# Kernel optimization log

Hardware: AMD Instinct MI355X
Metric: run time of the kernel (lower is better)

## Reference

```python
import jax, jax.numpy as jnp
import numpy as np

DIM = 768
NUM_HEADS = 12
HEAD_DIM = DIM // NUM_HEADS
SCALE = HEAD_DIM ** -0.5


def setup_inputs() -> dict:
    key = jax.random.key(0)
    k_x, k_qkv, k_proj, k_pb = jax.random.split(key, 4)
    B, N = 8, 1024
    x = jax.random.normal(k_x, (B, N, DIM), dtype=jnp.float32)
    # nn.Linear(dim, 3*dim, bias=False): weight [3*dim, dim]
    w_qkv = jax.random.normal(k_qkv, (3 * DIM, DIM), dtype=jnp.float32) * (DIM ** -0.5)
    # nn.Linear(dim, dim): weight [dim, dim], bias [dim]
    w_proj = jax.random.normal(k_proj, (DIM, DIM), dtype=jnp.float32) * (DIM ** -0.5)
    b_proj = jax.random.normal(k_pb, (DIM,), dtype=jnp.float32) * 0.01
    return {"x": x, "w_qkv": w_qkv, "w_proj": w_proj, "b_proj": b_proj}


def reference(x, w_qkv, w_proj, b_proj):
    B, N, C = x.shape
    H, D = NUM_HEADS, HEAD_DIM
    # qkv: [B, N, 3C] -> [3, B, H, N, D]
    qkv = jnp.einsum('bnc,oc->bno', x, w_qkv)
    qkv = qkv.reshape(B, N, 3, H, D).transpose(2, 0, 3, 1, 4)
    q, k, v = qkv[0], qkv[1], qkv[2]
    # scores in float32 (module explicitly casts to float)
    attn = jnp.einsum('bhnd,bhmd->bhnm', q.astype(jnp.float32), k.astype(jnp.float32)) * SCALE
    attn = jax.nn.softmax(attn, axis=-1)
    attn = jnp.where(jnp.isnan(attn), 0.0, attn)  # masked_fill nan -> 0
    out = jnp.einsum('bhnm,bhmd->bhnd', attn, v.astype(jnp.float32))
    out = out.transpose(0, 2, 1, 3).reshape(B, N, C)
    out = jnp.einsum('bnc,oc->bno', out, w_proj) + b_proj
    return out
```

## Files before the change

kernel.cpp:

```cpp
#include <hip/hip_runtime.h>

typedef _Float16 half8 __attribute__((ext_vector_type(8)));
typedef _Float16 half4 __attribute__((ext_vector_type(4)));
typedef float f32x4 __attribute__((ext_vector_type(4)));

#define NHEAD 12
#define HDIM  64
#define SEQ   1024
#define CDIM  768
#define O3    2304
#define MTOK  8192

__device__ __forceinline__ void load_lds16(const void* g, void* l) {
  __builtin_amdgcn_global_load_lds(
      (const __attribute__((address_space(1))) unsigned int*)g,
      (__attribute__((address_space(3))) unsigned int*)l, 16, 0, 0);
}

__global__ __launch_bounds__(256) void cast_f2h(const float* __restrict__ in,
                                                _Float16* __restrict__ out) {
  size_t i = ((size_t)blockIdx.x * 256 + threadIdx.x) * 4;
  float4 v = *reinterpret_cast<const float4*>(in + i);
  half4 h;
  h[0] = (_Float16)v.x; h[1] = (_Float16)v.y; h[2] = (_Float16)v.z; h[3] = (_Float16)v.w;
  *reinterpret_cast<half4*>(out + i) = h;
}

__global__ __launch_bounds__(256) void qkv_gemm(const _Float16* __restrict__ A,
                                                const _Float16* __restrict__ Bw,
                                                _Float16* __restrict__ Qh,
                                                _Float16* __restrict__ Kh,
                                                _Float16* __restrict__ VT) {
  __shared__ _Float16 As[2][128 * 32];
  __shared__ _Float16 Bs[2][128 * 32];
  const int tid  = threadIdx.x;
  const int lane = tid & 63;
  const int wv   = tid >> 6;
  const int wm   = wv >> 1;
  const int wn   = wv & 1;
  const int fr   = lane & 15;
  const int kg   = lane >> 4;

  const int lin = blockIdx.y * gridDim.x + blockIdx.x;
  const int cpx = (gridDim.x * gridDim.y) >> 3;
  const int swz = (lin & 7) * cpx + (lin >> 3);
  const int m0  = (swz / 18) * 128;
  const int n0  = (swz % 18) * 128;

  f32x4 acc[4][4];
#pragma unroll
  for (int i = 0; i < 4; ++i)
#pragma unroll
    for (int j = 0; j < 4; ++j) acc[i][j] = (f32x4){0.f, 0.f, 0.f, 0.f};

  auto stage = [&](int buf, int kt) {
#pragma unroll
    for (int r = 0; r < 2; ++r) {
      const int c = r * 256 + tid;
      const int row = c >> 2, cc = c & 3;
      load_lds16(A + (size_t)(m0 + row) * CDIM + kt + ((cc ^ (row & 3)) * 8),
                 &As[buf][c * 8]);
    }
#pragma unroll
    for (int r = 0; r < 2; ++r) {
      const int c = r * 256 + tid;
      const int row = c >> 2, cc = c & 3;
      load_lds16(Bw + (size_t)(n0 + row) * CDIM + kt + ((cc ^ (row & 3)) * 8),
                 &Bs[buf][c * 8]);
    }
  };

  int cur = 0;
  stage(0, 0);
  __syncthreads();

  for (int it = 0; it < 24; ++it) {
    if (it + 1 < 24) stage(cur ^ 1, (it + 1) * 32);
    half8 a[4], b[4];
#pragma unroll
    for (int i = 0; i < 4; ++i) {
      const int row = wm * 64 + i * 16 + fr;
      a[i] = *reinterpret_cast<half8*>(&As[cur][row * 32 + ((kg ^ (row & 3)) * 8)]);
    }
#pragma unroll
    for (int j = 0; j < 4; ++j) {
      const int row = wn * 64 + j * 16 + fr;
      b[j] = *reinterpret_cast<half8*>(&Bs[cur][row * 32 + ((kg ^ (row & 3)) * 8)]);
    }
#pragma unroll
    for (int i = 0; i < 4; ++i)
#pragma unroll
      for (int j = 0; j < 4; ++j)
        acc[i][j] = __builtin_amdgcn_mfma_f32_16x16x32_f16(a[i], b[j], acc[i][j], 0, 0, 0);
    if (it + 1 < 24) {
      __syncthreads();
      cur ^= 1;
    }
  }

  const int t     = n0 / CDIM;
  const int hbase = n0 - t * CDIM;
#pragma unroll
  for (int i = 0; i < 4; ++i) {
    const int mrow = m0 + wm * 64 + i * 16 + kg * 4;
#pragma unroll
    for (int j = 0; j < 4; ++j) {
      const int hd = hbase + wn * 64 + j * 16 + fr;
      const int h  = hd >> 6, d = hd & 63;
#pragma unroll
      for (int r = 0; r < 4; ++r) {
        const int m  = mrow + r;
        const int bb = m >> 10, nn = m & 1023;
        const float v = acc[i][j][r];
        if (t == 0)
          Qh[(((size_t)(bb * NHEAD + h)) << 16) + (nn << 6) + d] = (_Float16)(v * 0.125f);
        else if (t == 1)
          Kh[(((size_t)(bb * NHEAD + h)) << 16) + (nn << 6) + d] = (_Float16)v;
        else
          VT[(((size_t)(bb * NHEAD + h)) << 16) + (d << 10) + nn] = (_Float16)v;
      }
    }
  }
}

__global__ __launch_bounds__(256) void attn_kernel(const _Float16* __restrict__ Qh,
                                                   const _Float16* __restrict__ Kh,
                                                   const _Float16* __restrict__ VT,
                                                   _Float16* __restrict__ AO) {
  __shared__ _Float16 Ks[64 * 64];
  __shared__ _Float16 Vs[64 * 64];
  __shared__ _Float16 Ps[4 * 16 * 64];
  const int tid  = threadIdx.x;
  const int lane = tid & 63;
  const int w    = tid >> 6;
  const int fr   = lane & 15;
  const int kg   = lane >> 4;
  const int kh   = kg * 8;
  const int bh   = blockIdx.x;
  const int qt   = blockIdx.y;
  const int q0   = qt * 64 + w * 16;
  const size_t qkbase = (size_t)bh * SEQ * HDIM;
  char* const psw = (char*)&Ps[w * 16 * 64];

  half8 qb[2];
#pragma unroll
  for (int ks = 0; ks < 2; ++ks)
    qb[ks] = *reinterpret_cast<const half8*>(
        &Qh[qkbase + (size_t)(q0 + fr) * HDIM + ks * 32 + kh]);

  f32x4 O[4];
  float mrun = -__builtin_inff();
  float lrun = 0.f;
#pragma unroll
  for (int fd = 0; fd < 4; ++fd) O[fd] = (f32x4){0.f, 0.f, 0.f, 0.f};

  for (int kt = 0; kt < SEQ; kt += 64) {
    __syncthreads();
#pragma unroll
    for (int r = 0; r < 2; ++r) {
      const int c = r * 256 + tid;
      const int row = c >> 3, cc = c & 7;
      load_lds16(&Kh[qkbase + (size_t)(kt + row) * HDIM + ((cc ^ (row & 7)) * 8)], &Ks[c * 8]);
    }
#pragma unroll
    for (int r = 0; r < 2; ++r) {
      const int c = r * 256 + tid;
      const int row = c >> 3, cc = c & 7;
      load_lds16(&VT[(size_t)bh * HDIM * SEQ + (size_t)row * SEQ + kt + ((cc ^ (row & 7)) * 8)],
                 &Vs[c * 8]);
    }
    __syncthreads();

    f32x4 st[4];
#pragma unroll
    for (int fc = 0; fc < 4; ++fc) st[fc] = (f32x4){0.f, 0.f, 0.f, 0.f};
#pragma unroll
    for (int ks = 0; ks < 2; ++ks) {
#pragma unroll
      for (int fc = 0; fc < 4; ++fc) {
        const int row = fc * 16 + fr;
        const int colh = ks * 32 + kh;
        half8 ka = *reinterpret_cast<half8*>(&Ks[row * 64 + (((colh >> 3) ^ (row & 7)) << 3)]);
        st[fc] = __builtin_amdgcn_mfma_f32_16x16x32_f16(ka, qb[ks], st[fc], 0, 0, 0);
      }
    }

    float mx = st[0][0];
#pragma unroll
    for (int fc = 0; fc < 4; ++fc)
#pragma unroll
      for (int r = 0; r < 4; ++r) mx = fmaxf(mx, st[fc][r]);
    mx = fmaxf(mx, __shfl_xor(mx, 16));
    mx = fmaxf(mx, __shfl_xor(mx, 32));
    const float mnew = fmaxf(mrun, mx);
    const float corr = __expf(mrun - mnew);
    mrun = mnew;
    float rs = 0.f;
#pragma unroll
    for (int fc = 0; fc < 4; ++fc)
#pragma unroll
      for (int r = 0; r < 4; ++r) {
        const float p = __expf(st[fc][r] - mnew);
        st[fc][r] = p;
        rs += p;
      }
    rs += __shfl_xor(rs, 16);
    rs += __shfl_xor(rs, 32);
    lrun = lrun * corr + rs;

#pragma unroll
    for (int r = 0; r < 4; ++r) {
      const float c4 = __shfl(corr, kg * 4 + r);
#pragma unroll
      for (int fd = 0; fd < 4; ++fd) O[fd][r] *= c4;
    }

#pragma unroll
    for (int fc = 0; fc < 4; ++fc) {
      half4 pk;
      pk[0] = (_Float16)st[fc][0];
      pk[1] = (_Float16)st[fc][1];
      pk[2] = (_Float16)st[fc][2];
      pk[3] = (_Float16)st[fc][3];
      const int slot = (fc * 2 + (kg >> 1)) ^ (fr & 7);
      *reinterpret_cast<half4*>(psw + fr * 128 + slot * 16 + (kg & 1) * 8) = pk;
    }

#pragma unroll
    for (int ks = 0; ks < 2; ++ks) {
      const int rslot = (ks * 4 + kg) ^ (fr & 7);
      half8 pa = *reinterpret_cast<half8*>(psw + fr * 128 + rslot * 16);
#pragma unroll
      for (int fd = 0; fd < 4; ++fd) {
        const int row = fd * 16 + fr;
        const int colh = ks * 32 + kh;
        half8 vb = *reinterpret_cast<half8*>(&Vs[row * 64 + (((colh >> 3) ^ (row & 7)) << 3)]);
        O[fd] = __builtin_amdgcn_mfma_f32_16x16x32_f16(pa, vb, O[fd], 0, 0, 0);
      }
    }
  }

  const int b = bh / NHEAD, h = bh % NHEAD;
  const float linv = 1.0f / lrun;
#pragma unroll
  for (int r = 0; r < 4; ++r) {
    const float lq = __shfl(linv, kg * 4 + r);
    const int n = q0 + kg * 4 + r;
#pragma unroll
    for (int fd = 0; fd < 4; ++fd)
      AO[((size_t)b * SEQ + n) * CDIM + h * HDIM + fd * 16 + fr] =
          (_Float16)(O[fd][r] * lq);
  }
}

__global__ __launch_bounds__(256) void proj_gemm(const _Float16* __restrict__ A,
                                                 const _Float16* __restrict__ Bw,
                                                 const float* __restrict__ bias,
                                                 float* __restrict__ Out) {
  __shared__ _Float16 As[2][128 * 32];
  __shared__ _Float16 Bs[2][128 * 32];
  const int tid  = threadIdx.x;
  const int lane = tid & 63;
  const int wv   = tid >> 6;
  const int wm   = wv >> 1;
  const int wn   = wv & 1;
  const int fr   = lane & 15;
  const int kg   = lane >> 4;

  const int lin = blockIdx.y * gridDim.x + blockIdx.x;
  const int cpx = (gridDim.x * gridDim.y) >> 3;
  const int swz = (lin & 7) * cpx + (lin >> 3);
  const int m0  = (swz / 6) * 128;
  const int n0  = (swz % 6) * 128;

  f32x4 acc[4][4];
#pragma unroll
  for (int i = 0; i < 4; ++i)
#pragma unroll
    for (int j = 0; j < 4; ++j) acc[i][j] = (f32x4){0.f, 0.f, 0.f, 0.f};

  auto stage = [&](int buf, int kt) {
#pragma unroll
    for (int r = 0; r < 2; ++r) {
      const int c = r * 256 + tid;
      const int row = c >> 2, cc = c & 3;
      load_lds16(A + (size_t)(m0 + row) * CDIM + kt + ((cc ^ (row & 3)) * 8),
                 &As[buf][c * 8]);
    }
#pragma unroll
    for (int r = 0; r < 2; ++r) {
      const int c = r * 256 + tid;
      const int row = c >> 2, cc = c & 3;
      load_lds16(Bw + (size_t)(n0 + row) * CDIM + kt + ((cc ^ (row & 3)) * 8),
                 &Bs[buf][c * 8]);
    }
  };

  int cur = 0;
  stage(0, 0);
  __syncthreads();

  for (int it = 0; it < 24; ++it) {
    if (it + 1 < 24) stage(cur ^ 1, (it + 1) * 32);
    half8 a[4], b[4];
#pragma unroll
    for (int i = 0; i < 4; ++i) {
      const int row = wm * 64 + i * 16 + fr;
      a[i] = *reinterpret_cast<half8*>(&As[cur][row * 32 + ((kg ^ (row & 3)) * 8)]);
    }
#pragma unroll
    for (int j = 0; j < 4; ++j) {
      const int row = wn * 64 + j * 16 + fr;
      b[j] = *reinterpret_cast<half8*>(&Bs[cur][row * 32 + ((kg ^ (row & 3)) * 8)]);
    }
#pragma unroll
    for (int i = 0; i < 4; ++i)
#pragma unroll
      for (int j = 0; j < 4; ++j)
        acc[i][j] = __builtin_amdgcn_mfma_f32_16x16x32_f16(a[i], b[j], acc[i][j], 0, 0, 0);
    if (it + 1 < 24) {
      __syncthreads();
      cur ^= 1;
    }
  }

#pragma unroll
  for (int i = 0; i < 4; ++i) {
    const int mrow = m0 + wm * 64 + i * 16 + kg * 4;
#pragma unroll
    for (int j = 0; j < 4; ++j) {
      const int ocol = n0 + wn * 64 + j * 16 + fr;
      const float bv = bias[ocol];
#pragma unroll
      for (int r = 0; r < 4; ++r)
        Out[(size_t)(mrow + r) * CDIM + ocol] = acc[i][j][r] + bv;
    }
  }
}

extern "C" void kernel_launch(void* const* d_in, const int* in_sizes, int n_in,
                              void* d_out, int out_size, void* d_ws, size_t ws_size,
                              hipStream_t stream) {
  const float* x     = (const float*)d_in[0];
  const float* wqkv  = (const float*)d_in[1];
  const float* wproj = (const float*)d_in[2];
  const float* bproj = (const float*)d_in[3];
  float* out = (float*)d_out;

  char* ws = (char*)d_ws;
  _Float16* x_h     = (_Float16*)(ws);
  _Float16* wqkv_h  = (_Float16*)(ws + 12582912);
  _Float16* wproj_h = (_Float16*)(ws + 16121856);
  _Float16* Qh      = (_Float16*)(ws + 17301504);
  _Float16* Kh      = (_Float16*)(ws + 29884416);
  _Float16* VT      = (_Float16*)(ws + 42467328);
  _Float16* AOh     = (_Float16*)(ws + 55050240);

  cast_f2h<<<6291456 / 1024, 256, 0, stream>>>(x, x_h);
  cast_f2h<<<1769472 / 1024, 256, 0, stream>>>(wqkv, wqkv_h);
  cast_f2h<<<589824 / 1024, 256, 0, stream>>>(wproj, wproj_h);

  qkv_gemm<<<dim3(O3 / 128, MTOK / 128), 256, 0, stream>>>(x_h, wqkv_h, Qh, Kh, VT);
  attn_kernel<<<dim3(96, 16), 256, 0, stream>>>(Qh, Kh, VT, AOh);
  proj_gemm<<<dim3(CDIM / 128, MTOK / 128), 256, 0, stream>>>(AOh, wproj_h, bproj, out);
}
```

Before: 164.9 us.

## Double-buffer K/V tiles in attention and widen GEMM K-tiles to 64

The attention kernel now keeps two LDS buffers for K and V and loads the next tile while computing on the current one, where before every tile load was bracketed by barriers with no overlap. The QKV and projection GEMMs move from a 32-wide to a 64-wide K step with an 8-way XOR swizzle and named ping-pong buffers, which halves the number of barriers per output tile. This doubles LDS use per block in all three kernels, which may lower occupancy.

New measurement: 144.0 us. 12.7% less time.

```diff
diff --git a/kernel.cpp b/kernel.cpp
--- a/kernel.cpp
+++ b/kernel.cpp
@@ -31,8 +31,8 @@
                                                 _Float16* __restrict__ Qh,
                                                 _Float16* __restrict__ Kh,
                                                 _Float16* __restrict__ VT) {
-  __shared__ _Float16 As[2][128 * 32];
-  __shared__ _Float16 Bs[2][128 * 32];
+  __shared__ _Float16 As0[128 * 64], Bs0[128 * 64];
+  __shared__ _Float16 As1[128 * 64], Bs1[128 * 64];
   const int tid  = threadIdx.x;
   const int lane = tid & 63;
   const int wv   = tid >> 6;
@@ -53,49 +53,55 @@
 #pragma unroll
     for (int j = 0; j < 4; ++j) acc[i][j] = (f32x4){0.f, 0.f, 0.f, 0.f};
 
-  auto stage = [&](int buf, int kt) {
-#pragma unroll
-    for (int r = 0; r < 2; ++r) {
-      const int c = r * 256 + tid;
-      const int row = c >> 2, cc = c & 3;
-      load_lds16(A + (size_t)(m0 + row) * CDIM + kt + ((cc ^ (row & 3)) * 8),
-                 &As[buf][c * 8]);
-    }
-#pragma unroll
-    for (int r = 0; r < 2; ++r) {
-      const int c = r * 256 + tid;
-      const int row = c >> 2, cc = c & 3;
-      load_lds16(Bw + (size_t)(n0 + row) * CDIM + kt + ((cc ^ (row & 3)) * 8),
-                 &Bs[buf][c * 8]);
-    }
-  };
-
-  int cur = 0;
-  stage(0, 0);
+  auto stage = [&](_Float16* Ad, _Float16* Bd, int kt) {
+#pragma unroll
+    for (int r = 0; r < 4; ++r) {
+      const int c = r * 256 + tid;
+      const int row = c >> 3, cc = c & 7;
+      load_lds16(A + (size_t)(m0 + row) * CDIM + kt + ((cc ^ (row & 7)) * 8), Ad + c * 8);
+    }
+#pragma unroll
+    for (int r = 0; r < 4; ++r) {
+      const int c = r * 256 + tid;
+      const int row = c >> 3, cc = c & 7;
+      load_lds16(Bw + (size_t)(n0 + row) * CDIM + kt + ((cc ^ (row & 7)) * 8), Bd + c * 8);
+    }
+  };
+
+  auto compute = [&](const _Float16* As, const _Float16* Bs) {
+#pragma unroll
+    for (int kk = 0; kk < 2; ++kk) {
+      half8 a[4], b[4];
+#pragma unroll
+      for (int i = 0; i < 4; ++i) {
+        const int row = wm * 64 + i * 16 + fr;
+        a[i] = *reinterpret_cast<const half8*>(
+            &As[row * 64 + (((kk * 4 + kg) ^ (row & 7)) * 8)]);
+      }
+#pragma unroll
+      for (int j = 0; j < 4; ++j) {
+        const int row = wn * 64 + j * 16 + fr;
+        b[j] = *reinterpret_cast<const half8*>(
+            &Bs[row * 64 + (((kk * 4 + kg) ^ (row & 7)) * 8)]);
+      }
+#pragma unroll
+      for (int i = 0; i < 4; ++i)
+#pragma unroll
+        for (int j = 0; j < 4; ++j)
+          acc[i][j] = __builtin_amdgcn_mfma_f32_16x16x32_f16(a[i], b[j], acc[i][j], 0, 0, 0);
+    }
+  };
+
+  stage(As0, Bs0, 0);
   __syncthreads();
-
-  for (int it = 0; it < 24; ++it) {
-    if (it + 1 < 24) stage(cur ^ 1, (it + 1) * 32);
-    half8 a[4], b[4];
-#pragma unroll
-    for (int i = 0; i < 4; ++i) {
-      const int row = wm * 64 + i * 16 + fr;
-      a[i] = *reinterpret_cast<half8*>(&As[cur][row * 32 + ((kg ^ (row & 3)) * 8)]);
-    }
-#pragma unroll
-    for (int j = 0; j < 4; ++j) {
-      const int row = wn * 64 + j * 16 + fr;
-      b[j] = *reinterpret_cast<half8*>(&Bs[cur][row * 32 + ((kg ^ (row & 3)) * 8)]);
-    }
-#pragma unroll
-    for (int i = 0; i < 4; ++i)
-#pragma unroll
-      for (int j = 0; j < 4; ++j)
-        acc[i][j] = __builtin_amdgcn_mfma_f32_16x16x32_f16(a[i], b[j], acc[i][j], 0, 0, 0);
-    if (it + 1 < 24) {
-      __syncthreads();
-      cur ^= 1;
-    }
+  for (int it = 0; it < 6; ++it) {
+    const int kt = it * 128;
+    stage(As1, Bs1, kt + 64);
+    compute(As0, Bs0);
+    __syncthreads();
+    if (kt + 128 < CDIM) stage(As0, Bs0, kt + 128);
+    compute(As1, Bs1);
+    __syncthreads();
   }
 
   const int t     = n0 / CDIM;
@@ -127,8 +133,8 @@
                                                    const _Float16* __restrict__ Kh,
                                                    const _Float16* __restrict__ VT,
                                                    _Float16* __restrict__ AO) {
-  __shared__ _Float16 Ks[64 * 64];
-  __shared__ _Float16 Vs[64 * 64];
+  __shared__ _Float16 Ks0[64 * 64], Vs0[64 * 64];
+  __shared__ _Float16 Ks1[64 * 64], Vs1[64 * 64];
   __shared__ _Float16 Ps[4 * 16 * 64];
   const int tid  = threadIdx.x;
   const int lane = tid & 63;
@@ -154,23 +160,23 @@
 #pragma unroll
   for (int fd = 0; fd < 4; ++fd) O[fd] = (f32x4){0.f, 0.f, 0.f, 0.f};
 
-  for (int kt = 0; kt < SEQ; kt += 64) {
-    __syncthreads();
+  auto stageKV = [&](_Float16* Kd, _Float16* Vd, int kt) {
 #pragma unroll
     for (int r = 0; r < 2; ++r) {
       const int c = r * 256 + tid;
       const int row = c >> 3, cc = c & 7;
-      load_lds16(&Kh[qkbase + (size_t)(kt + row) * HDIM + ((cc ^ (row & 7)) * 8)], &Ks[c * 8]);
+      load_lds16(&Kh[qkbase + (size_t)(kt + row) * HDIM + ((cc ^ (row & 7)) * 8)], Kd + c * 8);
     }
 #pragma unroll
     for (int r = 0; r < 2; ++r) {
       const int c = r * 256 + tid;
       const int row = c >> 3, cc = c & 7;
       load_lds16(&VT[(size_t)bh * HDIM * SEQ + (size_t)row * SEQ + kt + ((cc ^ (row & 7)) * 8)],
-                 &Vs[c * 8]);
-    }
-    __syncthreads();
-
+                 Vd + c * 8);
+    }
+  };
+
+  auto computeKV = [&](const _Float16* Ksrc, const _Float16* Vsrc) {
     f32x4 st[4];
 #pragma unroll
     for (int fc = 0; fc < 4; ++fc) st[fc] = (f32x4){0.f, 0.f, 0.f, 0.f};
@@ -180,7 +186,8 @@
       for (int fc = 0; fc < 4; ++fc) {
         const int row = fc * 16 + fr;
         const int colh = ks * 32 + kh;
-        half8 ka = *reinterpret_cast<half8*>(&Ks[row * 64 + (((colh >> 3) ^ (row & 7)) << 3)]);
+        half8 ka = *reinterpret_cast<const half8*>(
+            &Ksrc[row * 64 + (((colh >> 3) ^ (row & 7)) << 3)]);
         st[fc] = __builtin_amdgcn_mfma_f32_16x16x32_f16(ka, qb[ks], st[fc], 0, 0, 0);
       }
     }
@@ -234,10 +241,23 @@
       for (int fd = 0; fd < 4; ++fd) {
         const int row = fd * 16 + fr;
         const int colh = ks * 32 + kh;
-        half8 vb = *reinterpret_cast<half8*>(&Vs[row * 64 + (((colh >> 3) ^ (row & 7)) << 3)]);
+        half8 vb = *reinterpret_cast<const half8*>(
+            &Vsrc[row * 64 + (((colh >> 3) ^ (row & 7)) << 3)]);
         O[fd] = __builtin_amdgcn_mfma_f32_16x16x32_f16(pa, vb, O[fd], 0, 0, 0);
       }
     }
+  };
+
+  stageKV(Ks0, Vs0, 0);
+  __syncthreads();
+  for (int it = 0; it < 8; ++it) {
+    const int kt = it * 128;
+    stageKV(Ks1, Vs1, kt + 64);
+    computeKV(Ks0, Vs0);
+    __syncthreads();
+    if (kt + 128 < SEQ) stageKV(Ks0, Vs0, kt + 128);
+    computeKV(Ks1, Vs1);
+    __syncthreads();
   }
 
   const int b = bh / NHEAD, h = bh % NHEAD;
@@ -257,8 +277,8 @@
                                                  const _Float16* __restrict__ Bw,
                                                  const float* __restrict__ bias,
                                                  float* __restrict__ Out) {
-  __shared__ _Float16 As[2][128 * 32];
-  __shared__ _Float16 Bs[2][128 * 32];
+  __shared__ _Float16 As0[128 * 64], Bs0[128 * 64];
+  __shared__ _Float16 As1[128 * 64], Bs1[128 * 64];
   const int tid  = threadIdx.x;
   const int lane = tid & 63;
   const int wv   = tid >> 6;
@@ -279,49 +299,55 @@
 #pragma unroll
     for (int j = 0; j < 4; ++j) acc[i][j] = (f32x4){0.f, 0.f, 0.f, 0.f};
 
-  auto stage = [&](int buf, int kt) {
-#pragma unroll
-    for (int r = 0; r < 2; ++r) {
-      const int c = r * 256 + tid;
-      const int row = c >> 2, cc = c & 3;
-      load_lds16(A + (size_t)(m0 + row) * CDIM + kt + ((cc ^ (row & 3)) * 8),
-                 &As[buf][c * 8]);
-    }
-#pragma unroll
-    for (int r = 0; r < 2; ++r) {
-      const int c = r * 256 + tid;
-      const int row = c >> 2, cc = c & 3;
-      load_lds16(Bw + (size_t)(n0 + row) * CDIM + kt + ((cc ^ (row & 3)) * 8),
-                 &Bs[buf][c * 8]);
-    }
-  };
-
-  int cur = 0;
-  stage(0, 0);
+  auto stage = [&](_Float16* Ad, _Float16* Bd, int kt) {
+#pragma unroll
+    for (int r = 0; r < 4; ++r) {
+      const int c = r * 256 + tid;
+      const int row = c >> 3, cc = c & 7;
+      load_lds16(A + (size_t)(m0 + row) * CDIM + kt + ((cc ^ (row & 7)) * 8), Ad + c * 8);
+    }
+#pragma unroll
+    for (int r = 0; r < 4; ++r) {
+      const int c = r * 256 + tid;
+      const int row = c >> 3, cc = c & 7;
+      load_lds16(Bw + (size_t)(n0 + row) * CDIM + kt + ((cc ^ (row & 7)) * 8), Bd + c * 8);
+    }
+  };
+
+  auto compute = [&](const _Float16* As, const _Float16* Bs) {
+#pragma unroll
+    for (int kk = 0; kk < 2; ++kk) {
+      half8 a[4], b[4];
+#pragma unroll
+      for (int i = 0; i < 4; ++i) {
+        const int row = wm * 64 + i * 16 + fr;
+        a[i] = *reinterpret_cast<const half8*>(
+            &As[row * 64 + (((kk * 4 + kg) ^ (row & 7)) * 8)]);
+      }
+#pragma unroll
+      for (int j = 0; j < 4; ++j) {
+        const int row = wn * 64 + j * 16 + fr;
+        b[j] = *reinterpret_cast<const half8*>(
+            &Bs[row * 64 + (((kk * 4 + kg) ^ (row & 7)) * 8)]);
+      }
+#pragma unroll
+      for (int i = 0; i < 4; ++i)
+#pragma unroll
+        for (int j = 0; j < 4; ++j)
+          acc[i][j] = __builtin_amdgcn_mfma_f32_16x16x32_f16(a[i], b[j], acc[i][j], 0, 0, 0);
+    }
+  };
+
+  stage(As0, Bs0, 0);
   __syncthreads();
-
-  for (int it = 0; it < 24; ++it) {
-    if (it + 1 < 24) stage(cur ^ 1, (it + 1) * 32);
-    half8 a[4], b[4];
-#pragma unroll
-    for (int i = 0; i < 4; ++i) {
-      const int row = wm * 64 + i * 16 + fr;
-      a[i] = *reinterpret_cast<half8*>(&As[cur][row * 32 + ((kg ^ (row & 3)) * 8)]);
-    }
-#pragma unroll
-    for (int j = 0; j < 4; ++j) {
-      const int row = wn * 64 + j * 16 + fr;
-      b[j] = *reinterpret_cast<half8*>(&Bs[cur][row * 32 + ((kg ^ (row & 3)) * 8)]);
-    }
-#pragma unroll
-    for (int i = 0; i < 4; ++i)
-#pragma unroll
-      for (int j = 0; j < 4; ++j)
-        acc[i][j] = __builtin_amdgcn_mfma_f32_16x16x32_f16(a[i], b[j], acc[i][j], 0, 0, 0);
-    if (it + 1 < 24) {
-      __syncthreads();
-      cur ^= 1;
-    }
+  for (int it = 0; it < 6; ++it) {
+    const int kt = it * 128;
+    stage(As1, Bs1, kt + 64);
+    compute(As0, Bs0);
+    __syncthreads();
+    if (kt + 128 < CDIM) stage(As0, Bs0, kt + 128);
+    compute(As1, Bs1);
+    __syncthreads();
   }
 
 #pragma unroll
```
